# Kernel tuning notes

Hardware: AMD Instinct MI355X
Metric: run time of the kernel (lower is better)

The kernel has to match this reference:

```python
import jax, jax.numpy as jnp
import numpy as np
from jax import lax

KD, KH, KW = 9, 9, 9  # box-filter window (matches torch ones([1,1,9,9,9]))


def _box_sum(x):
    """Sum over a 9x9x9 window with SAME (zero) padding, via separable 1D convs.
    x: [B, 1, D, H, W]. Mathematically identical to conv3d with an all-ones
    9x9x9 kernel, but O(3k) instead of O(k^3) work per voxel.
    """
    dn = ('NCDHW', 'OIDHW', 'NCDHW')
    dt = x.dtype
    kd = jnp.ones((1, 1, KD, 1, 1), dt)
    kh = jnp.ones((1, 1, 1, KH, 1), dt)
    kw = jnp.ones((1, 1, 1, 1, KW), dt)
    pd, ph, pw = (KD - 1) // 2, (KH - 1) // 2, (KW - 1) // 2
    x = lax.conv_general_dilated(x, kd, (1, 1, 1), [(pd, pd), (0, 0), (0, 0)], dimension_numbers=dn)
    x = lax.conv_general_dilated(x, kh, (1, 1, 1), [(0, 0), (ph, ph), (0, 0)], dimension_numbers=dn)
    x = lax.conv_general_dilated(x, kw, (1, 1, 1), [(0, 0), (0, 0), (pw, pw)], dimension_numbers=dn)
    return x


def setup_inputs() -> dict:
    key = jax.random.key(0)
    k1, k2 = jax.random.split(key)
    shape = (2, 1, 160, 192, 160)  # [B, C=1, D, H, W]
    return {
        'input': jax.random.normal(k1, shape, dtype=jnp.float32),
        'target': jax.random.normal(k2, shape, dtype=jnp.float32),
    }


def reference(input, target):
    ksize = jnp.asarray(KD * KH * KW, input.dtype)
    I_sum = _box_sum(input)
    T_sum = _box_sum(target)
    II_sum = _box_sum(input * input)
    TT_sum = _box_sum(target * target)
    IT_sum = _box_sum(input * target)

    Ihat = I_sum / ksize
    That = T_sum / ksize
    cross = IT_sum - Ihat * T_sum - That * I_sum + That * Ihat * ksize
    T_var = TT_sum - 2 * That * T_sum + That * That * ksize
    I_var = II_sum - 2 * Ihat * I_sum + Ihat * Ihat * ksize
    cc = cross * cross / (T_var * I_var + 1e-5)
    return -1.0 * jnp.mean(cc)
```

## Files before the change

kernel.cpp:

```cpp
#include <hip/hip_runtime.h>

#define DIM_W 160
#define DIM_H 192
#define DIM_D 160
#define DIM_B 2

constexpr int TW = 16;
constexpr int TH = 32;
constexpr int CH = 19;
constexpr int NCH = 9;
constexpr int RH = TH + 8;
constexpr float INV_K = 1.0f / 729.0f;
constexpr double NTOT = 9830400.0;

typedef unsigned int u32;
typedef __attribute__((address_space(1))) const u32 gu32;
typedef __attribute__((address_space(3))) u32 lu32;
typedef _Float16 h2 __attribute__((ext_vector_type(2)));

__global__ void init_kernel(float* out, float* ws) {
    out[0] = 0.0f;
    ws[0] = 0.0f; ws[1] = 0.0f; ws[2] = 0.0f; ws[3] = 0.0f;
}

__device__ __forceinline__ int clampD(int s) {
    return s < 0 ? 0 : (s > DIM_D - 1 ? DIM_D - 1 : s);
}

__device__ __forceinline__ u32 pkf16(float a, float b) {
    return __builtin_bit_cast(u32, __builtin_amdgcn_cvt_pkrtz(a, b));
}

__global__ __launch_bounds__(256)
void lncc3d_kernel(const float* __restrict__ I,
                   const float* __restrict__ T,
                   const float* __restrict__ zsrc,
                   float* __restrict__ out)
{
    __shared__ __align__(16) float sR[2][2][RH][32];
    __shared__ __align__(16) uint2 wA[RH][16];
    __shared__ __align__(16) float  wB[16][44];
    __shared__ float red[4];

    const int tid  = threadIdx.x;
    const int lane = tid & 63;
    const int wid  = tid >> 6;
    const int wo   = tid & 15;
    const int hb   = (tid >> 4) << 1;

    const int bw = blockIdx.x, bh = blockIdx.y, bz = blockIdx.z;
    const int b  = bz / NCH;
    const int c  = bz - b * NCH;
    const int w0 = bw * TW, h0 = bh * TH, d0 = c * CH;
    const int dEnd = min(d0 + CH, DIM_D);

    const int plane = DIM_H * DIM_W;
    const int fld  = wid >> 1;
    const int kodd = wid & 1;
    const int nck  = kodd ? 2 : 3;
    const float* Fb = (fld ? T : I) + (size_t)b * DIM_D * plane;

    int boff[3], crw[3];
#pragma unroll
    for (int i = 0; i < 3; ++i) {
        const int ck  = kodd ? (2 * i + 1) : (2 * i);
        const int row = 8 * ck + (lane >> 3);
        const int pf4 = lane & 7;
        const int lf4 = (pf4 - 2 * row) & 7;
        const int gh  = h0 - 4 + row;
        const int gw  = w0 - 8 + (lf4 << 2);
        crw[i]  = 8 * ck;
        boff[i] = (i < nck && gh >= 0 && gh < DIM_H && gw >= 0 && gw <= DIM_W - 4)
                  ? (gh * DIM_W + gw) : -1;
    }

    auto issue = [&](int sc, int buf) {
        const float* Fs = Fb + (size_t)sc * plane;
#pragma unroll
        for (int i = 0; i < 3; ++i) {
            if (i < nck) {
                const float* gp = (boff[i] >= 0) ? (Fs + boff[i]) : zsrc;
                __builtin_amdgcn_global_load_lds((gu32*)gp, (lu32*)&sR[buf][fld][crw[i]][0],
                                                 16, 0, 0);
            }
        }
    };

    float rgI[2][9], rgT[2][9], rgII[2][9], rgTT[2][9], rgIT[2][9];
    float rnI[2], rnT[2], rnII[2], rnTT[2], rnIT[2];
#pragma unroll
    for (int p = 0; p < 2; ++p) {
        rnI[p] = rnT[p] = rnII[p] = rnTT[p] = rnIT[p] = 0.0f;
#pragma unroll
        for (int q = 0; q < 9; ++q) {
            rgI[p][q] = rgT[p][q] = rgII[p][q] = rgTT[p][q] = rgIT[p][q] = 0.0f;
        }
    }
    float acc = 0.0f;

    const int sStart = d0 - 4;
    int cur = 0;

    issue(clampD(sStart), 0);
    issue(clampD(sStart + 1), 1);
    if (kodd) { asm volatile("s_waitcnt vmcnt(2)" ::: "memory"); }
    else      { asm volatile("s_waitcnt vmcnt(3)" ::: "memory"); }
    __builtin_amdgcn_s_barrier();

    for (int t = 0; t < 3; ++t) {
        const int t9 = t * 9;
#pragma unroll
        for (int j = 0; j < 9; ++j) {
            const int s  = sStart + t9 + j;
            const bool vs = (s >= 0) && (s < DIM_D);

            if (vs && tid < 160) {
                const int r = tid >> 2;
                const int g = tid & 3;
                const float* rIp = &sR[cur][0][r][0];
                const float* rTp = &sR[cur][1][r][0];
                const int q0 = ((g + 1 + 2 * r) & 7) << 2;
                const int q1 = ((g + 2 + 2 * r) & 7) << 2;
                const int q2 = ((g + 3 + 2 * r) & 7) << 2;
                const float4 ia  = *(const float4*)(rIp + q0);
                const float4 ib4 = *(const float4*)(rIp + q1);
                const float4 ic4 = *(const float4*)(rIp + q2);
                const float4 ta  = *(const float4*)(rTp + q0);
                const float4 tb4 = *(const float4*)(rTp + q1);
                const float4 tc4 = *(const float4*)(rTp + q2);
                const float iv[12] = {ia.x, ia.y, ia.z, ia.w, ib4.x, ib4.y, ib4.z, ib4.w,
                                      ic4.x, ic4.y, ic4.z, ic4.w};
                const float tv[12] = {ta.x, ta.y, ta.z, ta.w, tb4.x, tb4.y, tb4.z, tb4.w,
                                      tc4.x, tc4.y, tc4.z, tc4.w};
                float aI = 0.f, aT = 0.f, aII = 0.f, aTT = 0.f, aIT = 0.f;
#pragma unroll
                for (int k = 0; k < 9; ++k) {
                    aI += iv[k]; aT += tv[k];
                    aII = fmaf(iv[k], iv[k], aII);
                    aTT = fmaf(tv[k], tv[k], aTT);
                    aIT = fmaf(iv[k], tv[k], aIT);
                }
                const int c0 = g << 2;
                wA[r][(c0 + r) & 15] = make_uint2(pkf16(aI, aT), pkf16(aII, aTT));
                wB[c0][r] = aIT;
#pragma unroll
                for (int q = 1; q < 4; ++q) {
                    const float ni = iv[8 + q], oi = iv[q - 1];
                    const float nt = tv[8 + q], ot = tv[q - 1];
                    aI += ni - oi; aT += nt - ot;
                    aII = fmaf(ni, ni, fmaf(oi, -oi, aII));
                    aTT = fmaf(nt, nt, fmaf(ot, -ot, aTT));
                    aIT = fmaf(ni, nt, fmaf(oi, -ot, aIT));
                    wA[r][(c0 + q + r) & 15] = make_uint2(pkf16(aI, aT), pkf16(aII, aTT));
                    wB[c0 + q][r] = aIT;
                }
            }
            asm volatile("s_waitcnt lgkmcnt(0)" ::: "memory");
            __builtin_amdgcn_s_barrier();

            issue(clampD(s + 2), cur);

            float s2I0, s2T0, s2II0, s2TT0, s2IT0, s2I1, s2T1, s2II1, s2TT1, s2IT1;
            if (vs) {
                const uint2 C0 = wA[hb][(wo + hb) & 15];
                const h2 A0a = __builtin_bit_cast(h2, C0.x);
                const h2 A0b = __builtin_bit_cast(h2, C0.y);
                h2 SA = A0a, SB = A0b;
#pragma unroll
                for (int k = 1; k < 9; ++k) {
                    const uint2 Ck = wA[hb + k][(wo + hb + k) & 15];
                    SA += __builtin_bit_cast(h2, Ck.x);
                    SB += __builtin_bit_cast(h2, Ck.y);
                }
                const uint2 C9 = wA[hb + 9][(wo + hb + 9) & 15];
                const h2 P1A = SA - A0a + __builtin_bit_cast(h2, C9.x);
                const h2 P1B = SB - A0b + __builtin_bit_cast(h2, C9.y);
                s2I0  = (float)SA.x;  s2T0  = (float)SA.y;
                s2II0 = (float)SB.x;  s2TT0 = (float)SB.y;
                s2I1  = (float)P1A.x; s2T1  = (float)P1A.y;
                s2II1 = (float)P1B.x; s2TT1 = (float)P1B.y;
                const float2 B0 = *(const float2*)&wB[wo][hb];
                const float2 B1 = *(const float2*)&wB[wo][hb + 2];
                const float2 B2 = *(const float2*)&wB[wo][hb + 4];
                const float2 B3 = *(const float2*)&wB[wo][hb + 6];
                const float2 B4 = *(const float2*)&wB[wo][hb + 8];
                s2IT0 = B0.x + B0.y + B1.x + B1.y + B2.x + B2.y
                      + B3.x + B3.y + B4.x;
                s2IT1 = s2IT0 - B0.x + B4.y;
            } else {
                s2I0 = s2T0 = s2II0 = s2TT0 = s2IT0 = 0.f;
                s2I1 = s2T1 = s2II1 = s2TT1 = s2IT1 = 0.f;
            }

            rnI[0]  += s2I0  - rgI[0][j];  rgI[0][j]  = s2I0;
            rnT[0]  += s2T0  - rgT[0][j];  rgT[0][j]  = s2T0;
            rnII[0] += s2II0 - rgII[0][j]; rgII[0][j] = s2II0;
            rnTT[0] += s2TT0 - rgTT[0][j]; rgTT[0][j] = s2TT0;
            rnIT[0] += s2IT0 - rgIT[0][j]; rgIT[0][j] = s2IT0;
            rnI[1]  += s2I1  - rgI[1][j];  rgI[1][j]  = s2I1;
            rnT[1]  += s2T1  - rgT[1][j];  rgT[1][j]  = s2T1;
            rnII[1] += s2II1 - rgII[1][j]; rgII[1][j] = s2II1;
            rnTT[1] += s2TT1 - rgTT[1][j]; rgTT[1][j] = s2TT1;
            rnIT[1] += s2IT1 - rgIT[1][j]; rgIT[1][j] = s2IT1;

            if ((s >= d0 + 4) && ((s - 4) < dEnd)) {
                float cr, vv, tvv;
                cr  = rnIT[0] - rnI[0] * rnT[0] * INV_K;
                vv  = rnII[0] - rnI[0] * rnI[0] * INV_K;
                tvv = rnTT[0] - rnT[0] * rnT[0] * INV_K;
                acc += cr * cr * __builtin_amdgcn_rcpf(fmaf(tvv, vv, 1e-5f));
                cr  = rnIT[1] - rnI[1] * rnT[1] * INV_K;
                vv  = rnII[1] - rnI[1] * rnI[1] * INV_K;
                tvv = rnTT[1] - rnT[1] * rnT[1] * INV_K;
                acc += cr * cr * __builtin_amdgcn_rcpf(fmaf(tvv, vv, 1e-5f));
            }

            asm volatile("s_waitcnt lgkmcnt(0)" ::: "memory");
            if (kodd) { asm volatile("s_waitcnt vmcnt(2)" ::: "memory"); }
            else      { asm volatile("s_waitcnt vmcnt(3)" ::: "memory"); }
            __builtin_amdgcn_s_barrier();
            cur ^= 1;
        }
    }

#pragma unroll
    for (int off = 32; off > 0; off >>= 1) acc += __shfl_down(acc, off, 64);
    if (lane == 0) red[wid] = acc;
    __syncthreads();
    if (tid == 0) {
        const float bs = red[0] + red[1] + red[2] + red[3];
        atomicAdd(out, bs * (float)(-1.0 / NTOT));
    }
}

extern "C" void kernel_launch(void* const* d_in, const int* in_sizes, int n_in,
                              void* d_out, int out_size, void* d_ws, size_t ws_size,
                              hipStream_t stream) {
    const float* I = (const float*)d_in[0];
    const float* T = (const float*)d_in[1];
    float* out = (float*)d_out;
    float* ws  = (float*)d_ws;

    init_kernel<<<dim3(1), dim3(1), 0, stream>>>(out, ws);

    dim3 grid(DIM_W / TW, DIM_H / TH, DIM_B * NCH);
    dim3 block(256);
    lncc3d_kernel<<<grid, block, 0, stream>>>(I, T, ws, out);
}
```

Measured before the change: 83.47 us.

## Double H-tile to 64 rows with 512-thread blocks and unswizzled 24-wide smem rows

Raises the tile height from 32 to 64 rows and the block size to 512 threads, which cuts the fractional H-halo overhead (8 halo rows per 64 instead of per 32) and halves the number of blocks. The global-to-LDS load mapping is rebuilt: each wave now handles one or two 64-lane jobs covering a 6-float4-wide row (24 floats) with a 4-column halo, replacing the earlier 32-wide rotated swizzle layout. An explicit vmcnt(0) is added before the final reduction, and the reduction now covers 8 waves. The larger block uses more LDS and registers per block and gives fewer blocks for the GPU to schedule, which may lower occupancy or balance, and the flat 24-float row stride may bring LDS bank conflicts.

```diff
diff --git a/kernel.cpp b/kernel.cpp
--- a/kernel.cpp
+++ b/kernel.cpp
@@ -6,10 +6,12 @@
 #define DIM_B 2
 
 constexpr int TW = 16;
-constexpr int TH = 32;
+constexpr int TH = 64;
 constexpr int CH = 19;
 constexpr int NCH = 9;
-constexpr int RH = TH + 8;
+constexpr int RH = 72;
+constexpr int RWDS = 24;
+constexpr int RPAD = 1792;
 constexpr float INV_K = 1.0f / 729.0f;
 constexpr double NTOT = 9830400.0;
 
@@ -31,16 +33,16 @@
     return __builtin_bit_cast(u32, __builtin_amdgcn_cvt_pkrtz(a, b));
 }
 
-__global__ __launch_bounds__(256)
+__global__ __launch_bounds__(512)
 void lncc3d_kernel(const float* __restrict__ I,
                    const float* __restrict__ T,
                    const float* __restrict__ zsrc,
                    float* __restrict__ out)
 {
-    __shared__ __align__(16) float sR[2][2][RH][32];
+    __shared__ __align__(16) float sR[2][2][RPAD];
     __shared__ __align__(16) uint2 wA[RH][16];
-    __shared__ __align__(16) float  wB[16][44];
-    __shared__ float red[4];
+    __shared__ __align__(16) float wB[16][74];
+    __shared__ float red[8];
 
     const int tid  = threadIdx.x;
     const int lane = tid & 63;
@@ -55,33 +57,35 @@
     const int dEnd = min(d0 + CH, DIM_D);
 
     const int plane = DIM_H * DIM_W;
-    const int fld  = wid >> 1;
-    const int kodd = wid & 1;
-    const int nck  = kodd ? 2 : 3;
-    const float* Fb = (fld ? T : I) + (size_t)b * DIM_D * plane;
-
-    int boff[3], crw[3];
-#pragma unroll
-    for (int i = 0; i < 3; ++i) {
-        const int ck  = kodd ? (2 * i + 1) : (2 * i);
-        const int row = 8 * ck + (lane >> 3);
-        const int pf4 = lane & 7;
-        const int lf4 = (pf4 - 2 * row) & 7;
+    const float* Ib = I + (size_t)b * DIM_D * plane;
+    const float* Tb = T + (size_t)b * DIM_D * plane;
+
+    const int njobs = (wid < 6) ? 2 : 1;
+    int jfld[2], boff[2], ldof[2];
+#pragma unroll
+    for (int i = 0; i < 2; ++i) {
+        const int job = wid + 8 * i;
+        const int fld = job / 7;
+        const int sub = job - fld * 7;
+        const int s16 = sub * 64 + lane;
+        const int row = s16 / 6;
+        const int q   = s16 - row * 6;
         const int gh  = h0 - 4 + row;
-        const int gw  = w0 - 8 + (lf4 << 2);
-        crw[i]  = 8 * ck;
-        boff[i] = (i < nck && gh >= 0 && gh < DIM_H && gw >= 0 && gw <= DIM_W - 4)
+        const int gw  = w0 - 4 + (q << 2);
+        jfld[i] = fld;
+        ldof[i] = sub << 8;
+        boff[i] = (row < RH && gh >= 0 && gh < DIM_H && gw >= 0 && gw <= DIM_W - 4)
                   ? (gh * DIM_W + gw) : -1;
     }
 
     auto issue = [&](int sc, int buf) {
-        const float* Fs = Fb + (size_t)sc * plane;
-#pragma unroll
-        for (int i = 0; i < 3; ++i) {
-            if (i < nck) {
+#pragma unroll
+        for (int i = 0; i < 2; ++i) {
+            if (i < njobs) {
+                const float* Fs = (jfld[i] ? Tb : Ib) + (size_t)sc * plane;
                 const float* gp = (boff[i] >= 0) ? (Fs + boff[i]) : zsrc;
-                __builtin_amdgcn_global_load_lds((gu32*)gp, (lu32*)&sR[buf][fld][crw[i]][0],
-                                                 16, 0, 0);
+                __builtin_amdgcn_global_load_lds((gu32*)gp,
+                    (lu32*)&sR[buf][jfld[i]][ldof[i]], 16, 0, 0);
             }
         }
     };
@@ -103,8 +107,8 @@
 
     issue(clampD(sStart), 0);
     issue(clampD(sStart + 1), 1);
-    if (kodd) { asm volatile("s_waitcnt vmcnt(2)" ::: "memory"); }
-    else      { asm volatile("s_waitcnt vmcnt(3)" ::: "memory"); }
+    if (wid < 6) { asm volatile("s_waitcnt vmcnt(2)" ::: "memory"); }
+    else         { asm volatile("s_waitcnt vmcnt(1)" ::: "memory"); }
     __builtin_amdgcn_s_barrier();
 
     for (int t = 0; t < 3; ++t) {
@@ -114,20 +118,18 @@
             const int s  = sStart + t9 + j;
             const bool vs = (s >= 0) && (s < DIM_D);
 
-            if (vs && tid < 160) {
-                const int r = tid >> 2;
-                const int g = tid & 3;
-                const float* rIp = &sR[cur][0][r][0];
-                const float* rTp = &sR[cur][1][r][0];
-                const int q0 = ((g + 1 + 2 * r) & 7) << 2;
-                const int q1 = ((g + 2 + 2 * r) & 7) << 2;
-                const int q2 = ((g + 3 + 2 * r) & 7) << 2;
-                const float4 ia  = *(const float4*)(rIp + q0);
-                const float4 ib4 = *(const float4*)(rIp + q1);
-                const float4 ic4 = *(const float4*)(rIp + q2);
-                const float4 ta  = *(const float4*)(rTp + q0);
-                const float4 tb4 = *(const float4*)(rTp + q1);
-                const float4 tc4 = *(const float4*)(rTp + q2);
+            if (vs && tid < 288) {
+                const int r  = tid >> 2;
+                const int g  = tid & 3;
+                const int c0 = g << 2;
+                const float* rIp = &sR[cur][0][r * RWDS];
+                const float* rTp = &sR[cur][1][r * RWDS];
+                const float4 ia  = *(const float4*)(rIp + c0);
+                const float4 ib4 = *(const float4*)(rIp + c0 + 4);
+                const float4 ic4 = *(const float4*)(rIp + c0 + 8);
+                const float4 ta  = *(const float4*)(rTp + c0);
+                const float4 tb4 = *(const float4*)(rTp + c0 + 4);
+                const float4 tc4 = *(const float4*)(rTp + c0 + 8);
                 const float iv[12] = {ia.x, ia.y, ia.z, ia.w, ib4.x, ib4.y, ib4.z, ib4.w,
                                       ic4.x, ic4.y, ic4.z, ic4.w};
                 const float tv[12] = {ta.x, ta.y, ta.z, ta.w, tb4.x, tb4.y, tb4.z, tb4.w,
@@ -140,7 +142,6 @@
                     aTT = fmaf(tv[k], tv[k], aTT);
                     aIT = fmaf(iv[k], tv[k], aIT);
                 }
-                const int c0 = g << 2;
                 wA[r][(c0 + r) & 15] = make_uint2(pkf16(aI, aT), pkf16(aII, aTT));
                 wB[c0][r] = aIT;
 #pragma unroll
@@ -216,19 +217,23 @@
             }
 
             asm volatile("s_waitcnt lgkmcnt(0)" ::: "memory");
-            if (kodd) { asm volatile("s_waitcnt vmcnt(2)" ::: "memory"); }
-            else      { asm volatile("s_waitcnt vmcnt(3)" ::: "memory"); }
+            if (wid < 6) { asm volatile("s_waitcnt vmcnt(2)" ::: "memory"); }
+            else         { asm volatile("s_waitcnt vmcnt(1)" ::: "memory"); }
             __builtin_amdgcn_s_barrier();
             cur ^= 1;
         }
     }
+
+    asm volatile("s_waitcnt vmcnt(0)" ::: "memory");
 
 #pragma unroll
     for (int off = 32; off > 0; off >>= 1) acc += __shfl_down(acc, off, 64);
     if (lane == 0) red[wid] = acc;
     __syncthreads();
     if (tid == 0) {
-        const float bs = red[0] + red[1] + red[2] + red[3];
+        float bs = 0.0f;
+#pragma unroll
+        for (int k = 0; k < 8; ++k) bs += red[k];
         atomicAdd(out, bs * (float)(-1.0 / NTOT));
     }
 }
@@ -244,6 +249,6 @@
     init_kernel<<<dim3(1), dim3(1), 0, stream>>>(out, ws);
 
     dim3 grid(DIM_W / TW, DIM_H / TH, DIM_B * NCH);
-    dim3 block(256);
+    dim3 block(512);
     lncc3d_kernel<<<grid, block, 0, stream>>>(I, T, ws, out);
 }
```

Measured after the change: 85.47 us. +2.4%, slower.
